# Performance work log

Measured on AMD Instinct MI355X. Metric: run time of the kernel, lower is better.

The kernel has to match this reference:

```python
import jax, jax.numpy as jnp
import numpy as np

B, N_IN, D_IN = 2048, 49, 320
D = 768            # inner_dim
H = 8              # n_heads
DH = D // H        # head dim = 96
NQ = 8             # n_queries
D_OUT = 3072       # llama_hidden
EPS = 1e-5


def _ln(x, g, b):
    mu = jnp.mean(x, axis=-1, keepdims=True)
    var = jnp.mean(jnp.square(x - mu), axis=-1, keepdims=True)
    return (x - mu) * jax.lax.rsqrt(var + EPS) * g + b


def setup_inputs() -> dict:
    key = jax.random.key(0)
    ks = jax.random.split(key, 16)
    s = lambda k, shape, fan: jax.random.normal(k, shape, jnp.float32) * (1.0 / np.sqrt(fan))
    return {
        "features": jax.random.normal(ks[0], (B, N_IN, D_IN), jnp.float32),
        "input_proj_w": s(ks[1], (D, D_IN), D_IN),
        "input_proj_b": jnp.zeros((D,), jnp.float32),
        "queries": jax.random.normal(ks[2], (NQ, D), jnp.float32) * 0.02,
        "ln_q_g": jnp.ones((D,), jnp.float32), "ln_q_b": jnp.zeros((D,), jnp.float32),
        "ln_kv_g": jnp.ones((D,), jnp.float32), "ln_kv_b": jnp.zeros((D,), jnp.float32),
        "in_proj_w": s(ks[3], (3 * D, D), D),
        "in_proj_b": jnp.zeros((3 * D,), jnp.float32),
        "out_proj_w": s(ks[4], (D, D), D),
        "out_proj_b": jnp.zeros((D,), jnp.float32),
        "ln_ff_g": jnp.ones((D,), jnp.float32), "ln_ff_b": jnp.zeros((D,), jnp.float32),
        "ffn_w1": s(ks[5], (D, D), D), "ffn_b1": jnp.zeros((D,), jnp.float32),
        "ffn_w2": s(ks[6], (D, D), D), "ffn_b2": jnp.zeros((D,), jnp.float32),
        "output_proj_w": s(ks[7], (D_OUT, D), D),
        "output_proj_b": jnp.zeros((D_OUT,), jnp.float32),
        "final_g": jnp.ones((D_OUT,), jnp.float32), "final_b": jnp.zeros((D_OUT,), jnp.float32),
    }


def reference(features, input_proj_w, input_proj_b, queries,
              ln_q_g, ln_q_b, ln_kv_g, ln_kv_b,
              in_proj_w, in_proj_b, out_proj_w, out_proj_b,
              ln_ff_g, ln_ff_b, ffn_w1, ffn_b1, ffn_w2, ffn_b2,
              output_proj_w, output_proj_b, final_g, final_b):
    b = features.shape[0]
    # kv projection: (B, N_in, D)
    kv = jnp.einsum('bnd,ed->bne', features, input_proj_w) + input_proj_b
    q = jnp.broadcast_to(queries[None], (b, NQ, D))

    # --- single layer (n_layers=1) ---
    q_norm = _ln(q, ln_q_g, ln_q_b)
    kv_norm = _ln(kv, ln_kv_g, ln_kv_b)

    wq, wk, wv = in_proj_w[:D], in_proj_w[D:2 * D], in_proj_w[2 * D:]
    bq, bk, bv = in_proj_b[:D], in_proj_b[D:2 * D], in_proj_b[2 * D:]
    qp = (jnp.einsum('bqd,ed->bqe', q_norm, wq) + bq).reshape(b, NQ, H, DH)
    kp = (jnp.einsum('bnd,ed->bne', kv_norm, wk) + bk).reshape(b, N_IN, H, DH)
    vp = (jnp.einsum('bnd,ed->bne', kv_norm, wv) + bv).reshape(b, N_IN, H, DH)

    scores = jnp.einsum('bqhd,bnhd->bhqn', qp, kp) / np.sqrt(DH).astype(np.float32)
    attn = jax.nn.softmax(scores, axis=-1)
    ctx = jnp.einsum('bhqn,bnhd->bqhd', attn, vp).reshape(b, NQ, D)
    attn_out = jnp.einsum('bqd,ed->bqe', ctx, out_proj_w) + out_proj_b

    q = q + attn_out
    h = _ln(q, ln_ff_g, ln_ff_b)
    h = jnp.einsum('bqd,ed->bqe', h, ffn_w1) + ffn_b1
    h = jax.nn.gelu(h, approximate=False)
    h = jnp.einsum('bqd,ed->bqe', h, ffn_w2) + ffn_b2
    q = q + h

    out = jnp.einsum('bqd,ed->bqe', q, output_proj_w) + output_proj_b
    return _ln(out, final_g, final_b)
```

## Files before the change

### kernel.cpp

```cpp
#include <hip/hip_runtime.h>
#include <math.h>

typedef __attribute__((ext_vector_type(8))) short short8;
typedef __attribute__((ext_vector_type(8))) unsigned short ushort8;
typedef __attribute__((ext_vector_type(4))) float f32x4;

__device__ __forceinline__ float b2f(unsigned short h) {
    union { unsigned int u; float f; } c; c.u = ((unsigned int)h) << 16; return c.f;
}
__device__ __forceinline__ unsigned short f2b(float x) {
    union { float f; unsigned int u; } c; c.f = x;
    unsigned int r = c.u + 0x7fffu + ((c.u >> 16) & 1u);
    return (unsigned short)(r >> 16);
}

__global__ __launch_bounds__(256) void cast_all(
    const float* __restrict__ f,    unsigned short* __restrict__ fb,
    const float* __restrict__ winw, unsigned short* __restrict__ winb,
    const float* __restrict__ wv,   unsigned short* __restrict__ wvb,
    const float* __restrict__ wo,   unsigned short* __restrict__ wob,
    const float* __restrict__ w1,   unsigned short* __restrict__ w1b,
    const float* __restrict__ w2,   unsigned short* __restrict__ w2b,
    const float* __restrict__ wop,  unsigned short* __restrict__ wopb,
    const float* __restrict__ gff) {
    int blk = blockIdx.x;
    const float* src; unsigned short* dst; int i;
    if (blk < 31360)      { src = f;    dst = fb;   i = blk * 256 + threadIdx.x; }
    else if (blk < 31600) { src = winw; dst = winb; i = (blk - 31360) * 256 + threadIdx.x; }
    else if (blk < 32176) { src = wv;   dst = wvb;  i = (blk - 31600) * 256 + threadIdx.x; }
    else if (blk < 32752) { src = wo;   dst = wob;  i = (blk - 32176) * 256 + threadIdx.x; }
    else if (blk < 33328) { src = w1;   dst = w1b;  i = (blk - 32752) * 256 + threadIdx.x; }
    else if (blk < 33904) { src = w2;   dst = w2b;  i = (blk - 33328) * 256 + threadIdx.x; }
    else                  { src = wop;  dst = wopb; i = (blk - 33904) * 256 + threadIdx.x; }
    float4 fv = ((const float4*)src)[i];
    if (blk >= 32752 && blk < 33328) {
        float4 g4 = ((const float4*)gff)[i % 192];
        fv.x *= g4.x; fv.y *= g4.y; fv.z *= g4.z; fv.w *= g4.w;
    }
    ushort4 o; o.x = f2b(fv.x); o.y = f2b(fv.y); o.z = f2b(fv.z); o.w = f2b(fv.w);
    ((ushort4*)dst)[i] = o;
}

template <int DD, bool INB, bool OUTB>
__global__ __launch_bounds__(256) void ln_rows(const void* __restrict__ in_, void* __restrict__ out_,
                                               const float* __restrict__ g, const float* __restrict__ bb,
                                               int nrows) {
    const int wv = threadIdx.x >> 6, l = threadIdx.x & 63;
    const int row = blockIdx.x * 4 + wv;
    if (row >= nrows) return;
    constexpr int NC = DD / 256;
    float v[DD / 64];
    if constexpr (INB) {
        const ushort4* in = (const ushort4*)((const unsigned short*)in_ + (size_t)row * DD);
#pragma unroll
        for (int c = 0; c < NC; ++c) {
            ushort4 u = in[l + 64 * c];
            v[4*c] = b2f(u.x); v[4*c+1] = b2f(u.y); v[4*c+2] = b2f(u.z); v[4*c+3] = b2f(u.w);
        }
    } else {
        const float4* in = (const float4*)((const float*)in_ + (size_t)row * DD);
#pragma unroll
        for (int c = 0; c < NC; ++c) {
            float4 u = in[l + 64 * c];
            v[4*c] = u.x; v[4*c+1] = u.y; v[4*c+2] = u.z; v[4*c+3] = u.w;
        }
    }
    float s = 0.f, s2 = 0.f;
#pragma unroll
    for (int i = 0; i < DD / 64; ++i) { s += v[i]; s2 += v[i] * v[i]; }
#pragma unroll
    for (int o = 32; o > 0; o >>= 1) { s += __shfl_xor(s, o, 64); s2 += __shfl_xor(s2, o, 64); }
    const float mu = s * (1.0f / DD);
    const float var = s2 * (1.0f / DD) - mu * mu;
    const float rs = rsqrtf(var + 1e-5f);
    if constexpr (OUTB) {
        ushort4* out = (ushort4*)((unsigned short*)out_ + (size_t)row * DD);
#pragma unroll
        for (int c = 0; c < NC; ++c) {
            int e = (l + 64 * c) * 4;
            ushort4 o4;
            o4.x = f2b((v[4*c]   - mu) * rs * g[e]   + bb[e]);
            o4.y = f2b((v[4*c+1] - mu) * rs * g[e+1] + bb[e+1]);
            o4.z = f2b((v[4*c+2] - mu) * rs * g[e+2] + bb[e+2]);
            o4.w = f2b((v[4*c+3] - mu) * rs * g[e+3] + bb[e+3]);
            out[l + 64 * c] = o4;
        }
    } else {
        float4* out = (float4*)((float*)out_ + (size_t)row * DD);
#pragma unroll
        for (int c = 0; c < NC; ++c) {
            int e = (l + 64 * c) * 4;
            float4 o4;
            o4.x = (v[4*c]   - mu) * rs * g[e]   + bb[e];
            o4.y = (v[4*c+1] - mu) * rs * g[e+1] + bb[e+1];
            o4.z = (v[4*c+2] - mu) * rs * g[e+2] + bb[e+2];
            o4.w = (v[4*c+3] - mu) * rs * g[e+3] + bb[e+3];
            out[l + 64 * c] = o4;
        }
    }
}

__global__ __launch_bounds__(256) void ln_stats(const unsigned short* __restrict__ m,
                                                float2* __restrict__ stats, int nrows) {
    const int wv = threadIdx.x >> 6, l = threadIdx.x & 63;
    const int row = blockIdx.x * 4 + wv;
    if (row >= nrows) return;
    const ushort4* in = (const ushort4*)(m + (size_t)row * 768);
    float s = 0.f, s2 = 0.f;
#pragma unroll
    for (int c = 0; c < 3; ++c) {
        ushort4 u = in[l + 64 * c];
        float a = b2f(u.x), b = b2f(u.y), cc = b2f(u.z), d = b2f(u.w);
        s += a + b + cc + d;
        s2 += a * a + b * b + cc * cc + d * d;
    }
#pragma unroll
    for (int o = 32; o > 0; o >>= 1) { s += __shfl_xor(s, o, 64); s2 += __shfl_xor(s2, o, 64); }
    const float mu = s * (1.0f / 768.0f);
    const float var = s2 * (1.0f / 768.0f) - mu * mu;
    const float rs = rsqrtf(var + 1e-5f);
    if (l == 0) stats[row] = make_float2(rs, rs * mu);
}

__global__ __launch_bounds__(256) void qp_kernel(const float* __restrict__ qn, const float* __restrict__ wq,
                                                 const float* __restrict__ bq, float* __restrict__ qp) {
    int q = blockIdx.x / 3;
    int col = (blockIdx.x % 3) * 256 + threadIdx.x;
    const float4* a = (const float4*)(qn + q * 768);
    const float4* wr = (const float4*)(wq + (size_t)col * 768);
    float s = 0.f;
#pragma unroll 8
    for (int k = 0; k < 192; ++k) {
        float4 xx = a[k], yy = wr[k];
        s += xx.x * yy.x + xx.y * yy.y + xx.z * yy.z + xx.w * yy.w;
    }
    qp[q * 768 + col] = s + bq[col];
}

__global__ __launch_bounds__(256) void qk_build(const float* __restrict__ qp, const float* __restrict__ wk,
                                                const float* __restrict__ g,
                                                unsigned short* __restrict__ qkg, float* __restrict__ tout) {
    __shared__ float red[4];
    const int hq = blockIdx.x, h = hq >> 3, q = hq & 7;
    const int tid = threadIdx.x;
    const float* qv = qp + q * 768 + h * 96;
    float tsum = 0.f;
#pragma unroll
    for (int c = 0; c < 3; ++c) {
        int e = tid + 256 * c;
        float s = 0.f;
        for (int d = 0; d < 96; ++d) s += qv[d] * wk[(size_t)(h * 96 + d) * 768 + e];
        unsigned short bv = f2b(s * 0.10206207262f * g[e]);
        qkg[hq * 768 + e] = bv;
        tsum += b2f(bv);
    }
#pragma unroll
    for (int o = 32; o > 0; o >>= 1) tsum += __shfl_xor(tsum, o, 64);
    if ((tid & 63) == 0) red[tid >> 6] = tsum;
    __syncthreads();
    if (tid == 0) tout[hq] = red[0] + red[1] + red[2] + red[3];
}

__global__ __launch_bounds__(256) void t1c1_build(const float* __restrict__ w1, const float* __restrict__ g,
                                                  const float* __restrict__ beta, const float* __restrict__ b1,
                                                  float* __restrict__ tvec, float* __restrict__ fb1) {
    int col = blockIdx.x * 256 + threadIdx.x;
    const float4* wr = (const float4*)(w1 + (size_t)col * 768);
    const float4* g4 = (const float4*)g;
    const float4* be = (const float4*)beta;
    float st = 0.f, sc = 0.f;
#pragma unroll 8
    for (int k = 0; k < 192; ++k) {
        float4 w = wr[k], gg = g4[k], bb = be[k];
        st += w.x * gg.x + w.y * gg.y + w.z * gg.z + w.w * gg.w;
        sc += w.x * bb.x + w.y * bb.y + w.z * bb.z + w.w * bb.w;
    }
    tvec[col] = st;
    fb1[col] = sc + b1[col];
}

__device__ __forceinline__ void gll16(const void* g, void* l) {
    __builtin_amdgcn_global_load_lds((const __attribute__((address_space(1))) unsigned int*)g,
                                     (__attribute__((address_space(3))) unsigned int*)l, 16, 0, 0);
}

template <int ROWS>
__device__ __forceinline__ void stage_rows(const unsigned short* gbase, int ldg,
                                           unsigned short* lds, int tid) {
    int wuni = tid & ~63;
#pragma unroll
    for (int it = 0; it < ROWS / 32; ++it) {
        int s = it * 256 + tid;
        int r = s >> 3, c = s & 7;
        int cc = c ^ (r & 7);
        gll16(gbase + (size_t)r * ldg + cc * 8, lds + (size_t)(it * 256 + wuni) * 8);
    }
}

template <int EPI>
__global__ __launch_bounds__(256) void gemm_bf16(
    const unsigned short* __restrict__ A, const unsigned short* __restrict__ W,
    const float* __restrict__ bias, void* __restrict__ out,
    const void* __restrict__ aux, const float2* __restrict__ rstats,
    const float* __restrict__ tvec, int K, int N, int CG) {
    __shared__ __align__(16) unsigned short lA[128 * 64];
    __shared__ __align__(16) unsigned short lB[128 * 64];
    const int tid = threadIdx.x;
    const int l = tid & 63, w = tid >> 6;
    int gx = gridDim.x, gy = gridDim.y;
    int lid = blockIdx.y * gx + blockIdx.x;
    int nwg = gx * gy;
    int bm0, bn0;
    if ((nwg & 7) || (gy & 7)) {
        bm0 = (lid / gx) * 128; bn0 = (lid % gx) * 128;
    } else {
        int xcd = lid & 7, loc = lid >> 3;
        int rpx = gy >> 3;
        int perg = rpx * CG;
        int cg = loc / perg, rem = loc % perg;
        bm0 = (xcd * rpx + rem / CG) * 128;
        bn0 = (cg * CG + rem % CG) * 128;
    }
    const int wm = (w >> 1) * 64, wn = (w & 1) * 64;
    const int l15 = l & 15, lk = l >> 4;
    f32x4 acc[4][4] = {};
    const int nk = K >> 6;
    const unsigned short* Abase = A + (size_t)bm0 * K;
    const unsigned short* Wbase = W + (size_t)bn0 * K;
    for (int kt = 0; kt < nk; ++kt) {
        stage_rows<128>(Abase + kt * 64, K, lA, tid);
        stage_rows<128>(Wbase + kt * 64, K, lB, tid);
        __syncthreads();
        short8 af[4], bf[4];
#pragma unroll
        for (int kk = 0; kk < 2; ++kk) {
#pragma unroll
            for (int mf = 0; mf < 4; ++mf) {
                int r = wm + mf * 16 + l15;
                int c = (kk * 4 + lk) ^ (r & 7);
                af[mf] = *(const short8*)(lA + r * 64 + c * 8);
            }
#pragma unroll
            for (int nf = 0; nf < 4; ++nf) {
                int r = wn + nf * 16 + l15;
                int c = (kk * 4 + lk) ^ (r & 7);
                bf[nf] = *(const short8*)(lB + r * 64 + c * 8);
            }
#pragma unroll
            for (int mf = 0; mf < 4; ++mf)
#pragma unroll
                for (int nf = 0; nf < 4; ++nf)
                    acc[mf][nf] = __builtin_amdgcn_mfma_f32_16x16x32_bf16(af[mf], bf[nf], acc[mf][nf], 0, 0, 0);
        }
        __syncthreads();
    }
    const int row0 = bm0 + wm + (lk << 2);
    const int col0 = bn0 + wn + l15;
    float bv[4], tv[4];
#pragma unroll
    for (int nf = 0; nf < 4; ++nf) {
        bv[nf] = bias[col0 + nf * 16];
        if constexpr (EPI == 2) tv[nf] = tvec[col0 + nf * 16];
    }
#pragma unroll
    for (int mf = 0; mf < 4; ++mf) {
#pragma unroll
        for (int r = 0; r < 4; ++r) {
            int row = row0 + mf * 16 + r;
            float rs = 0.f, u = 0.f;
            if constexpr (EPI == 2) {
                float2 st = rstats[row];
                rs = st.x; u = st.y;
            }
#pragma unroll
            for (int nf = 0; nf < 4; ++nf) {
                int col = col0 + nf * 16;
                size_t idx2 = (size_t)row * N + col;
                float v = acc[mf][nf][r];
                if constexpr (EPI == 0) {
                    v += bv[nf];
                } else if constexpr (EPI == 1) {
                    v += bv[nf] + ((const float*)aux)[(row & 7) * N + col];
                } else if constexpr (EPI == 2) {
                    v = rs * v - u * tv[nf] + bv[nf];
                    v = 0.5f * v * (1.0f + erff(v * 0.70710678118f));
                } else {
                    v += bv[nf] + b2f(((const unsigned short*)aux)[idx2]);
                }
                ((unsigned short*)out)[idx2] = f2b(v);
            }
        }
    }
}

__global__ __launch_bounds__(256) void gemm_scores(const unsigned short* __restrict__ A,
                                                   const unsigned short* __restrict__ Qk,
                                                   const float2* __restrict__ stats,
                                                   const float* __restrict__ tcol,
                                                   float* __restrict__ S) {
    __shared__ __align__(16) unsigned short lA[128 * 64];
    __shared__ __align__(16) unsigned short lB[64 * 64];
    const int tid = threadIdx.x;
    const int l = tid & 63, w = tid >> 6;
    int lid = blockIdx.x;
    int idx = (lid & 7) * (gridDim.x >> 3) + (lid >> 3);
    const int bm0 = idx * 128;
    const int wm = (w >> 1) * 64, wn = (w & 1) * 32;
    const int l15 = l & 15, lk = l >> 4;
    f32x4 acc[4][2] = {};
    const unsigned short* Abase = A + (size_t)bm0 * 768;
    for (int kt = 0; kt < 12; ++kt) {
        stage_rows<128>(Abase + kt * 64, 768, lA, tid);
        stage_rows<64>(Qk + kt * 64, 768, lB, tid);
        __syncthreads();
        short8 af[4], bf[2];
#pragma unroll
        for (int kk = 0; kk < 2; ++kk) {
#pragma unroll
            for (int mf = 0; mf < 4; ++mf) {
                int r = wm + mf * 16 + l15;
                int c = (kk * 4 + lk) ^ (r & 7);
                af[mf] = *(const short8*)(lA + r * 64 + c * 8);
            }
#pragma unroll
            for (int nf = 0; nf < 2; ++nf) {
                int r = wn + nf * 16 + l15;
                int c = (kk * 4 + lk) ^ (r & 7);
                bf[nf] = *(const short8*)(lB + r * 64 + c * 8);
            }
#pragma unroll
            for (int mf = 0; mf < 4; ++mf)
#pragma unroll
                for (int nf = 0; nf < 2; ++nf)
                    acc[mf][nf] = __builtin_amdgcn_mfma_f32_16x16x32_bf16(af[mf], bf[nf], acc[mf][nf], 0, 0, 0);
        }
        __syncthreads();
    }
    const int row0 = bm0 + wm + (lk << 2);
    const int col0 = wn + l15;
    const float tv0 = tcol[col0], tv1 = tcol[col0 + 16];
#pragma unroll
    for (int mf = 0; mf < 4; ++mf)
#pragma unroll
        for (int r = 0; r < 4; ++r) {
            int row = row0 + mf * 16 + r;
            float2 st = stats[row];
            S[(size_t)row * 64 + col0]      = st.x * acc[mf][0][r] - st.y * tv0;
            S[(size_t)row * 64 + col0 + 16] = st.x * acc[mf][1][r] - st.y * tv1;
        }
}

__global__ __launch_bounds__(256) void attn_mix(const unsigned short* __restrict__ kvr,
                                                const float* __restrict__ S,
                                                const float2* __restrict__ stats,
                                                const float* __restrict__ lg,
                                                const float* __restrict__ lb,
                                                unsigned short* __restrict__ cmix) {
    __shared__ __align__(16) unsigned short at[64 * 64];
    __shared__ __align__(16) unsigned short kvT[128 * 64];
    __shared__ float dl[64];
    __shared__ float2 sst[49];
    float* Sl = (float*)kvT;
    const int b = blockIdx.x;
    const int t = threadIdx.x, l = t & 63, w = t >> 6;
    const int l15 = l & 15, lk = l >> 4;

    for (int i = t; i < 3136; i += 256) Sl[i] = S[(size_t)b * 3136 + i];
    if (t < 49) sst[t] = stats[(size_t)b * 49 + t];

    const unsigned short* src = kvr + ((size_t)b * 49 + (l < 49 ? l : 0)) * 768;
    ushort8 z8 = {0, 0, 0, 0, 0, 0, 0, 0};
    ushort8 va0 = z8, va1 = z8, va2 = z8, va3 = z8;
    if (l < 49) {
        va0 = *(const ushort8*)(src + w * 8);
        va1 = *(const ushort8*)(src + w * 8 + 32);
        va2 = *(const ushort8*)(src + w * 8 + 64);
        va3 = *(const ushort8*)(src + w * 8 + 96);
    }
    __syncthreads();

    float mx = -1e30f;
    for (int n = 0; n < 49; ++n) mx = fmaxf(mx, Sl[n * 64 + l]);
    float sum = 0.f, dun = 0.f;
    for (int n = 0; n < 49; ++n) {
        float e = __expf(Sl[n * 64 + l] - mx);
        sum += e;
        dun += e * sst[n].y;
    }
    float inv = 1.0f / sum;
#pragma unroll
    for (int cd = 0; cd < 2; ++cd) {
        int c = w * 2 + cd;
        int cc = c ^ (l & 7);
#pragma unroll
        for (int j = 0; j < 8; ++j) {
            int n = c * 8 + j;
            float av = 0.f;
            if (n < 49) av = __expf(Sl[n * 64 + l] - mx) * inv * sst[n].x;
            at[l * 64 + cc * 8 + j] = f2b(av);
        }
    }
    if (w == 0) dl[l] = dun * inv;
    __syncthreads();

    float dls[4];
#pragma unroll
    for (int nf = 0; nf < 4; ++nf) dls[nf] = dl[nf * 16 + l15];

#pragma unroll 1
    for (int ph = 0; ph < 6; ++ph) {
#pragma unroll
        for (int i = 0; i < 4; ++i) {
            ushort8 v = (i == 0) ? va0 : (i == 1) ? va1 : (i == 2) ? va2 : va3;
            int e0 = w * 8 + i * 32;
#pragma unroll
            for (int j = 0; j < 8; ++j) {
                int e = e0 + j;
                kvT[e * 64 + (((l >> 3) ^ (e & 7)) << 3) + (l & 7)] = v[j];
            }
        }
        ushort8 nb0 = z8, nb1 = z8, nb2 = z8, nb3 = z8;
        if (ph < 5 && l < 49) {
            const unsigned short* s2 = src + (ph + 1) * 128 + w * 8;
            nb0 = *(const ushort8*)(s2);
            nb1 = *(const ushort8*)(s2 + 32);
            nb2 = *(const ushort8*)(s2 + 64);
            nb3 = *(const ushort8*)(s2 + 96);
        }
        __syncthreads();
        f32x4 acc[2][4] = {};
#pragma unroll
        for (int ks = 0; ks < 2; ++ks) {
            short8 af[2], bf[4];
#pragma unroll
            for (int mf = 0; mf < 2; ++mf) {
                int r = w * 32 + mf * 16 + l15;
                af[mf] = *(const short8*)(kvT + r * 64 + (((ks * 4 + lk) ^ (r & 7)) << 3));
            }
#pragma unroll
            for (int nf = 0; nf < 4; ++nf) {
                int r = nf * 16 + l15;
                bf[nf] = *(const short8*)(at + r * 64 + (((ks * 4 + lk) ^ (r & 7)) << 3));
            }
#pragma unroll
            for (int mf = 0; mf < 2; ++mf)
#pragma unroll
                for (int nf = 0; nf < 4; ++nf)
                    acc[mf][nf] = __builtin_amdgcn_mfma_f32_16x16x32_bf16(af[mf], bf[nf], acc[mf][nf], 0, 0, 0);
        }
#pragma unroll
        for (int mf = 0; mf < 2; ++mf) {
            int e0 = ph * 128 + w * 32 + mf * 16 + lk * 4;
            float4 g4 = *(const float4*)(lg + e0);
            float4 b4 = *(const float4*)(lb + e0);
#pragma unroll
            for (int nf = 0; nf < 4; ++nf) {
                int hq = nf * 16 + l15;
                float dv = dls[nf];
                ushort4 o;
                o.x = f2b(g4.x * (acc[mf][nf][0] - dv) + b4.x);
                o.y = f2b(g4.y * (acc[mf][nf][1] - dv) + b4.y);
                o.z = f2b(g4.z * (acc[mf][nf][2] - dv) + b4.z);
                o.w = f2b(g4.w * (acc[mf][nf][3] - dv) + b4.w);
                *(ushort4*)(cmix + ((size_t)(hq >> 3) * 16384 + b * 8 + (hq & 7)) * 768 + e0) = o;
            }
        }
        va0 = nb0; va1 = nb1; va2 = nb2; va3 = nb3;
        __syncthreads();
    }
}

__global__ __launch_bounds__(256) void gemm_ctx(const unsigned short* __restrict__ cmix,
                                                const unsigned short* __restrict__ wvb,
                                                const float* __restrict__ bv,
                                                unsigned short* __restrict__ ctx) {
    __shared__ __align__(16) unsigned short lA[128 * 64];
    __shared__ __align__(16) unsigned short lB[128 * 64];
    const int tid = threadIdx.x;
    const int l = tid & 63, w = tid >> 6;
    const int h = blockIdx.z;
    int yy = blockIdx.y;
    int idx = (yy & 7) * 16 + (yy >> 3);
    const int bm0 = idx * 128;
    const int wm = (w >> 1) * 64, wn = (w & 1) * 64;
    const int l15 = l & 15, lk = l >> 4;
    f32x4 acc[4][4] = {};
    const unsigned short* Abase = cmix + (size_t)h * 16384 * 768 + (size_t)bm0 * 768;
    const unsigned short* Wbase = wvb + (size_t)h * 96 * 768;
    for (int kt = 0; kt < 12; ++kt) {
        stage_rows<128>(Abase + kt * 64, 768, lA, tid);
        stage_rows<128>(Wbase + kt * 64, 768, lB, tid);
        __syncthreads();
        short8 af[4], bf[4];
#pragma unroll
        for (int kk = 0; kk < 2; ++kk) {
#pragma unroll
            for (int mf = 0; mf < 4; ++mf) {
                int r = wm + mf * 16 + l15;
                int c = (kk * 4 + lk) ^ (r & 7);
                af[mf] = *(const short8*)(lA + r * 64 + c * 8);
            }
#pragma unroll
            for (int nf = 0; nf < 4; ++nf) {
                int r = wn + nf * 16 + l15;
                int c = (kk * 4 + lk) ^ (r & 7);
                bf[nf] = *(const short8*)(lB + r * 64 + c * 8);
            }
#pragma unroll
            for (int mf = 0; mf < 4; ++mf)
#pragma unroll
                for (int nf = 0; nf < 4; ++nf)
                    acc[mf][nf] = __builtin_amdgcn_mfma_f32_16x16x32_bf16(af[mf], bf[nf], acc[mf][nf], 0, 0, 0);
        }
        __syncthreads();
    }
    const int row0 = bm0 + wm + (lk << 2);
    const int col0 = wn + l15;
#pragma unroll
    for (int nf = 0; nf < 4; ++nf) {
        int col = col0 + nf * 16;
        if (col >= 96) continue;
        float bvv = bv[h * 96 + col];
#pragma unroll
        for (int mf = 0; mf < 4; ++mf)
#pragma unroll
            for (int r = 0; r < 4; ++r) {
                int row = row0 + mf * 16 + r;
                ctx[(size_t)row * 768 + h * 96 + col] = f2b(acc[mf][nf][r] + bvv);
            }
    }
}

extern "C" void kernel_launch(void* const* d_in, const int* in_sizes, int n_in,
                              void* d_out, int out_size, void* d_ws, size_t ws_size,
                              hipStream_t stream) {
    (void)in_sizes; (void)n_in; (void)out_size;
    const float* features      = (const float*)d_in[0];
    const float* input_proj_w  = (const float*)d_in[1];
    const float* input_proj_b  = (const float*)d_in[2];
    const float* queries       = (const float*)d_in[3];
    const float* ln_q_g        = (const float*)d_in[4];
    const float* ln_q_b        = (const float*)d_in[5];
    const float* ln_kv_g       = (const float*)d_in[6];
    const float* ln_kv_b       = (const float*)d_in[7];
    const float* in_proj_w     = (const float*)d_in[8];
    const float* in_proj_b     = (const float*)d_in[9];
    const float* out_proj_w    = (const float*)d_in[10];
    const float* out_proj_b    = (const float*)d_in[11];
    const float* ln_ff_g       = (const float*)d_in[12];
    const float* ln_ff_b       = (const float*)d_in[13];
    const float* ffn_w1        = (const float*)d_in[14];
    const float* ffn_b1        = (const float*)d_in[15];
    const float* ffn_w2        = (const float*)d_in[16];
    const float* ffn_b2        = (const float*)d_in[17];
    const float* output_proj_w = (const float*)d_in[18];
    const float* output_proj_b = (const float*)d_in[19];
    const float* final_g       = (const float*)d_in[20];
    const float* final_b       = (const float*)d_in[21];

    char* ws = (char*)d_ws;
    size_t off = 0;
    auto alloc = [&](size_t bytes) -> char* {
        char* r = ws + off; off += (bytes + 255) & ~(size_t)255; return r;
    };
    unsigned short* featb = (unsigned short*)alloc(100352ull * 320 * 2);
    unsigned short* kvbuf = (unsigned short*)alloc(100352ull * 768 * 2);
    unsigned short* cmix  = (unsigned short*)alloc(8ull * 16384 * 768 * 2);
    float*          S     = (float*)alloc(100352ull * 64 * 4);
    float2*         kvst  = (float2*)alloc(100352ull * 8);
    float2*         xst   = (float2*)alloc(16384ull * 8);
    unsigned short* winb  = (unsigned short*)alloc(768ull * 320 * 2);
    unsigned short* wvb   = (unsigned short*)alloc(768ull * 768 * 2);
    unsigned short* woutb = (unsigned short*)alloc(768ull * 768 * 2);
    unsigned short* w1gb  = (unsigned short*)alloc(768ull * 768 * 2);
    unsigned short* w2b   = (unsigned short*)alloc(768ull * 768 * 2);
    unsigned short* wopb  = (unsigned short*)alloc(3072ull * 768 * 2);
    float* qnorm          = (float*)alloc(8 * 768 * 4);
    float* qpb            = (float*)alloc(8 * 768 * 4);
    unsigned short* qkb   = (unsigned short*)alloc(64ull * 768 * 2);
    float* tbuf           = (float*)alloc(64 * 4);
    float* t1vec          = (float*)alloc(768 * 4);
    float* fb1            = (float*)alloc(768 * 4);
    if (off > ws_size) return;

    unsigned short* ctx  = featb;
    unsigned short* outb = kvbuf;
    unsigned short* xb   = (unsigned short*)cmix;
    unsigned short* f1   = (unsigned short*)((char*)cmix + 25165824);
    unsigned short* x2   = (unsigned short*)((char*)cmix + 50331648);

    cast_all<<<36208, 256, 0, stream>>>(features, featb, input_proj_w, winb,
                                        in_proj_w + 2 * 768 * 768, wvb, out_proj_w, woutb,
                                        ffn_w1, w1gb, ffn_w2, w2b, output_proj_w, wopb, ln_ff_g);

    ln_rows<768, false, false><<<2, 256, 0, stream>>>(queries, qnorm, ln_q_g, ln_q_b, 8);
    qp_kernel<<<24, 256, 0, stream>>>(qnorm, in_proj_w, in_proj_b, qpb);
    qk_build<<<64, 256, 0, stream>>>(qpb, in_proj_w + 768 * 768, ln_kv_g, qkb, tbuf);
    t1c1_build<<<3, 256, 0, stream>>>(ffn_w1, ln_ff_g, ln_ff_b, ffn_b1, t1vec, fb1);

    gemm_bf16<0><<<dim3(6, 784), 256, 0, stream>>>(featb, winb, input_proj_b, kvbuf,
                                                   nullptr, nullptr, nullptr, 320, 768, 6);
    ln_stats<<<25088, 256, 0, stream>>>(kvbuf, kvst, 100352);
    gemm_scores<<<784, 256, 0, stream>>>(kvbuf, qkb, kvst, tbuf, S);
    attn_mix<<<2048, 256, 0, stream>>>(kvbuf, S, kvst, ln_kv_g, ln_kv_b, cmix);
    gemm_ctx<<<dim3(1, 128, 8), 256, 0, stream>>>(cmix, wvb, in_proj_b + 1536, ctx);
    gemm_bf16<1><<<dim3(6, 128), 256, 0, stream>>>(ctx, woutb, out_proj_b, xb,
                                                   queries, nullptr, nullptr, 768, 768, 6);
    ln_stats<<<4096, 256, 0, stream>>>(xb, xst, 16384);
    gemm_bf16<2><<<dim3(6, 128), 256, 0, stream>>>(xb, w1gb, fb1, f1,
                                                   nullptr, xst, t1vec, 768, 768, 6);
    gemm_bf16<3><<<dim3(6, 128), 256, 0, stream>>>(f1, w2b, ffn_b2, x2,
                                                   xb, nullptr, nullptr, 768, 768, 6);
    gemm_bf16<0><<<dim3(24, 128), 256, 0, stream>>>(x2, wopb, output_proj_b, outb,
                                                    nullptr, nullptr, nullptr, 768, 3072, 12);
    ln_rows<3072, true, false><<<4096, 256, 0, stream>>>(outb, (float*)d_out, final_g, final_b, 16384);
}
```

Measured before the change: 759.2 us.

## Fold input projection into score query vectors and split attn_mix across two blocks

Precomputes Qk·W_in so the score GEMM reads the 320-wide bf16 features instead of the 768-wide projected kv, cutting its K loop from 12 to 5 tiles. The bias contribution is added back through a per-column constant in the epilogue. A small qw_build kernel is added to do this folding. attn_mix now launches two blocks per batch, each covering three of the six head-chunk phases, which doubles parallelism but duplicates the softmax/stat setup work in each block. The extra bf16 rounding of the folded weights may shift numerics slightly.

```diff
diff --git a/kernel.cpp b/kernel.cpp
--- a/kernel.cpp
+++ b/kernel.cpp
@@ -138,13 +138,14 @@
 }
 
 __global__ __launch_bounds__(256) void qk_build(const float* __restrict__ qp, const float* __restrict__ wk,
-                                                const float* __restrict__ g,
-                                                unsigned short* __restrict__ qkg, float* __restrict__ tout) {
-    __shared__ float red[4];
+                                                const float* __restrict__ g, const float* __restrict__ ipb,
+                                                unsigned short* __restrict__ qkg,
+                                                float* __restrict__ tout, float* __restrict__ cout) {
+    __shared__ float red[4], red2[4];
     const int hq = blockIdx.x, h = hq >> 3, q = hq & 7;
     const int tid = threadIdx.x;
     const float* qv = qp + q * 768 + h * 96;
-    float tsum = 0.f;
+    float tsum = 0.f, csum = 0.f;
 #pragma unroll
     for (int c = 0; c < 3; ++c) {
         int e = tid + 256 * c;
@@ -152,13 +153,32 @@
         for (int d = 0; d < 96; ++d) s += qv[d] * wk[(size_t)(h * 96 + d) * 768 + e];
         unsigned short bv = f2b(s * 0.10206207262f * g[e]);
         qkg[hq * 768 + e] = bv;
-        tsum += b2f(bv);
-    }
-#pragma unroll
-    for (int o = 32; o > 0; o >>= 1) tsum += __shfl_xor(tsum, o, 64);
-    if ((tid & 63) == 0) red[tid >> 6] = tsum;
+        float bb = b2f(bv);
+        tsum += bb;
+        csum += ipb[e] * bb;
+    }
+#pragma unroll
+    for (int o = 32; o > 0; o >>= 1) {
+        tsum += __shfl_xor(tsum, o, 64);
+        csum += __shfl_xor(csum, o, 64);
+    }
+    if ((tid & 63) == 0) { red[tid >> 6] = tsum; red2[tid >> 6] = csum; }
     __syncthreads();
-    if (tid == 0) tout[hq] = red[0] + red[1] + red[2] + red[3];
+    if (tid == 0) {
+        tout[hq] = red[0] + red[1] + red[2] + red[3];
+        cout[hq] = red2[0] + red2[1] + red2[2] + red2[3];
+    }
+}
+
+__global__ __launch_bounds__(320) void qw_build(const unsigned short* __restrict__ qkg,
+                                                const float* __restrict__ ipw,
+                                                unsigned short* __restrict__ qwb) {
+    const int hq = blockIdx.x, kf = threadIdx.x;
+    const unsigned short* qr = qkg + hq * 768;
+    float s = 0.f;
+#pragma unroll 8
+    for (int e = 0; e < 768; ++e) s += b2f(qr[e]) * ipw[(size_t)e * 320 + kf];
+    qwb[hq * 320 + kf] = f2b(s);
 }
 
 __global__ __launch_bounds__(256) void t1c1_build(const float* __restrict__ w1, const float* __restrict__ g,
@@ -294,9 +314,10 @@
 }
 
 __global__ __launch_bounds__(256) void gemm_scores(const unsigned short* __restrict__ A,
-                                                   const unsigned short* __restrict__ Qk,
+                                                   const unsigned short* __restrict__ Qw,
                                                    const float2* __restrict__ stats,
                                                    const float* __restrict__ tcol,
+                                                   const float* __restrict__ ccol,
                                                    float* __restrict__ S) {
     __shared__ __align__(16) unsigned short lA[128 * 64];
     __shared__ __align__(16) unsigned short lB[64 * 64];
@@ -308,10 +329,10 @@
     const int wm = (w >> 1) * 64, wn = (w & 1) * 32;
     const int l15 = l & 15, lk = l >> 4;
     f32x4 acc[4][2] = {};
-    const unsigned short* Abase = A + (size_t)bm0 * 768;
-    for (int kt = 0; kt < 12; ++kt) {
-        stage_rows<128>(Abase + kt * 64, 768, lA, tid);
-        stage_rows<64>(Qk + kt * 64, 768, lB, tid);
+    const unsigned short* Abase = A + (size_t)bm0 * 320;
+    for (int kt = 0; kt < 5; ++kt) {
+        stage_rows<128>(Abase + kt * 64, 320, lA, tid);
+        stage_rows<64>(Qw + kt * 64, 320, lB, tid);
         __syncthreads();
         short8 af[4], bf[2];
 #pragma unroll
@@ -339,14 +360,15 @@
     const int row0 = bm0 + wm + (lk << 2);
     const int col0 = wn + l15;
     const float tv0 = tcol[col0], tv1 = tcol[col0 + 16];
+    const float cv0 = ccol[col0], cv1 = ccol[col0 + 16];
 #pragma unroll
     for (int mf = 0; mf < 4; ++mf)
 #pragma unroll
         for (int r = 0; r < 4; ++r) {
             int row = row0 + mf * 16 + r;
             float2 st = stats[row];
-            S[(size_t)row * 64 + col0]      = st.x * acc[mf][0][r] - st.y * tv0;
-            S[(size_t)row * 64 + col0 + 16] = st.x * acc[mf][1][r] - st.y * tv1;
+            S[(size_t)row * 64 + col0]      = st.x * (acc[mf][0][r] + cv0) - st.y * tv0;
+            S[(size_t)row * 64 + col0 + 16] = st.x * (acc[mf][1][r] + cv1) - st.y * tv1;
         }
 }
 
@@ -361,7 +383,9 @@
     __shared__ float dl[64];
     __shared__ float2 sst[49];
     float* Sl = (float*)kvT;
-    const int b = blockIdx.x;
+    const int half = blockIdx.x;
+    const int b = blockIdx.y;
+    const int ph0 = half * 3;
     const int t = threadIdx.x, l = t & 63, w = t >> 6;
     const int l15 = l & 15, lk = l >> 4;
 
@@ -372,10 +396,11 @@
     ushort8 z8 = {0, 0, 0, 0, 0, 0, 0, 0};
     ushort8 va0 = z8, va1 = z8, va2 = z8, va3 = z8;
     if (l < 49) {
-        va0 = *(const ushort8*)(src + w * 8);
-        va1 = *(const ushort8*)(src + w * 8 + 32);
-        va2 = *(const ushort8*)(src + w * 8 + 64);
-        va3 = *(const ushort8*)(src + w * 8 + 96);
+        const unsigned short* s0 = src + ph0 * 128 + w * 8;
+        va0 = *(const ushort8*)(s0);
+        va1 = *(const ushort8*)(s0 + 32);
+        va2 = *(const ushort8*)(s0 + 64);
+        va3 = *(const ushort8*)(s0 + 96);
     }
     __syncthreads();
 
@@ -408,7 +433,7 @@
     for (int nf = 0; nf < 4; ++nf) dls[nf] = dl[nf * 16 + l15];
 
 #pragma unroll 1
-    for (int ph = 0; ph < 6; ++ph) {
+    for (int ph = ph0; ph < ph0 + 3; ++ph) {
 #pragma unroll
         for (int i = 0; i < 4; ++i) {
             ushort8 v = (i == 0) ? va0 : (i == 1) ? va1 : (i == 2) ? va2 : va3;
@@ -420,7 +445,7 @@
             }
         }
         ushort8 nb0 = z8, nb1 = z8, nb2 = z8, nb3 = z8;
-        if (ph < 5 && l < 49) {
+        if (ph < ph0 + 2 && l < 49) {
             const unsigned short* s2 = src + (ph + 1) * 128 + w * 8;
             nb0 = *(const ushort8*)(s2);
             nb1 = *(const ushort8*)(s2 + 32);
@@ -578,7 +603,9 @@
     float* qnorm          = (float*)alloc(8 * 768 * 4);
     float* qpb            = (float*)alloc(8 * 768 * 4);
     unsigned short* qkb   = (unsigned short*)alloc(64ull * 768 * 2);
+    unsigned short* qwb   = (unsigned short*)alloc(64ull * 320 * 2);
     float* tbuf           = (float*)alloc(64 * 4);
+    float* cbuf           = (float*)alloc(64 * 4);
     float* t1vec          = (float*)alloc(768 * 4);
     float* fb1            = (float*)alloc(768 * 4);
     if (off > ws_size) return;
@@ -595,14 +622,15 @@
 
     ln_rows<768, false, false><<<2, 256, 0, stream>>>(queries, qnorm, ln_q_g, ln_q_b, 8);
     qp_kernel<<<24, 256, 0, stream>>>(qnorm, in_proj_w, in_proj_b, qpb);
-    qk_build<<<64, 256, 0, stream>>>(qpb, in_proj_w + 768 * 768, ln_kv_g, qkb, tbuf);
+    qk_build<<<64, 256, 0, stream>>>(qpb, in_proj_w + 768 * 768, ln_kv_g, input_proj_b, qkb, tbuf, cbuf);
+    qw_build<<<64, 320, 0, stream>>>(qkb, input_proj_w, qwb);
     t1c1_build<<<3, 256, 0, stream>>>(ffn_w1, ln_ff_g, ln_ff_b, ffn_b1, t1vec, fb1);
 
     gemm_bf16<0><<<dim3(6, 784), 256, 0, stream>>>(featb, winb, input_proj_b, kvbuf,
                                                    nullptr, nullptr, nullptr, 320, 768, 6);
     ln_stats<<<25088, 256, 0, stream>>>(kvbuf, kvst, 100352);
-    gemm_scores<<<784, 256, 0, stream>>>(kvbuf, qkb, kvst, tbuf, S);
-    attn_mix<<<2048, 256, 0, stream>>>(kvbuf, S, kvst, ln_kv_g, ln_kv_b, cmix);
+    gemm_scores<<<784, 256, 0, stream>>>(featb, qwb, kvst, tbuf, cbuf, S);
+    attn_mix<<<dim3(2, 2048), 256, 0, stream>>>(kvbuf, S, kvst, ln_kv_g, ln_kv_b, cmix);
     gemm_ctx<<<dim3(1, 128, 8), 256, 0, stream>>>(cmix, wvb, in_proj_b + 1536, ctx);
     gemm_bf16<1><<<dim3(6, 128), 256, 0, stream>>>(ctx, woutb, out_proj_b, xb,
                                                    queries, nullptr, nullptr, 768, 768, 6);
```

Result: slower. 801.0 us (+5.5%).
